# Kernel tuning notes

Measured on AMD Instinct MI355X. Metric: run time of the kernel, lower is better.

## Reference

```python
import jax, jax.numpy as jnp
import numpy as np

N_NODES = 100000
N_EDGES = 1600000
IN_DIM = 64
HIDDEN = 128
N_CLASSES = 16


def setup_inputs() -> dict:
    key = jax.random.key(0)
    ks = jax.random.split(key, 16)
    inp = {
        'feats': jax.random.normal(ks[0], (N_NODES, IN_DIM), dtype=jnp.float32),
        'H1_src': jax.random.randint(ks[1], (N_EDGES,), 0, N_NODES),
        'H1_dst': jax.random.randint(ks[2], (N_EDGES,), 0, N_NODES),
        'H2_src': jax.random.randint(ks[3], (N_EDGES,), 0, N_NODES),
        'H2_dst': jax.random.randint(ks[4], (N_EDGES,), 0, N_NODES),
        'W1_self1': 0.1 * jax.random.normal(ks[5], (IN_DIM, HIDDEN), dtype=jnp.float32),
        'W1_neigh1': 0.1 * jax.random.normal(ks[6], (IN_DIM, HIDDEN), dtype=jnp.float32),
        'W1_self2': 0.1 * jax.random.normal(ks[7], (HIDDEN, HIDDEN), dtype=jnp.float32),
        'W1_neigh2': 0.1 * jax.random.normal(ks[8], (HIDDEN, HIDDEN), dtype=jnp.float32),
        'W1_lin': 0.1 * jax.random.normal(ks[9], (HIDDEN, N_CLASSES), dtype=jnp.float32),
        'W2_self1': 0.1 * jax.random.normal(ks[10], (IN_DIM, HIDDEN), dtype=jnp.float32),
        'W2_neigh1': 0.1 * jax.random.normal(ks[11], (IN_DIM, HIDDEN), dtype=jnp.float32),
        'W2_self2': 0.1 * jax.random.normal(ks[12], (HIDDEN, HIDDEN), dtype=jnp.float32),
        'W2_neigh2': 0.1 * jax.random.normal(ks[13], (HIDDEN, HIDDEN), dtype=jnp.float32),
        'W2_lin': 0.1 * jax.random.normal(ks[14], (HIDDEN, N_CLASSES), dtype=jnp.float32),
    }
    return inp


def _neighbor_mean(x, src, dst, n_nodes):
    # gather messages along edges, sum into destinations, divide by in-degree
    msg = x[src]                                        # [E, d] irregular gather
    agg = jax.ops.segment_sum(msg, dst, num_segments=n_nodes)  # [N, d]
    deg = jax.ops.segment_sum(jnp.ones((src.shape[0],), x.dtype), dst,
                              num_segments=n_nodes)     # [N]
    return agg / jnp.maximum(deg, 1.0)[:, None]         # zero-degree nodes -> 0


def _sage_layer(x, src, dst, W_self, W_neigh):
    h_neigh = _neighbor_mean(x, src, dst, x.shape[0])
    return jax.nn.relu(x @ W_self + h_neigh @ W_neigh)


def _graphsage(src, dst, x, Ws1, Wn1, Ws2, Wn2, Wlin):
    h = _sage_layer(x, src, dst, Ws1, Wn1)
    h = _sage_layer(h, src, dst, Ws2, Wn2)
    graph_rep = jnp.mean(h, axis=0)                     # dgl.mean_nodes (single graph)
    return jax.nn.sigmoid(graph_rep @ Wlin)             # [num_classes]


def reference(feats, H1_src, H1_dst, H2_src, H2_dst,
              W1_self1, W1_neigh1, W1_self2, W1_neigh2, W1_lin,
              W2_self1, W2_neigh1, W2_self2, W2_neigh2, W2_lin):
    rep1 = _graphsage(H1_src, H1_dst, feats, W1_self1, W1_neigh1, W1_self2, W1_neigh2, W1_lin)
    rep2 = _graphsage(H2_src, H2_dst, feats, W2_self1, W2_neigh1, W2_self2, W2_neigh2, W2_lin)
    return (rep1 + rep2) / 2.0
```

## Files before the change

### kernel.cpp

```cpp
#include <hip/hip_runtime.h>
#include <hip/hip_fp16.h>

#define NN 100000
#define NE 1600000
#define IND 64
#define HID 128
#define NCLS 16
#define NGRP 3125
#define RBLK 125
#define NCRS 98
#define CAPC 18432
#define CAPF 656
#define NDCAP 48
#define EPB1 8192
#define NBG1 ((NE + EPB1 - 1) / EPB1)
#define FSPLIT 4
#define FSPAN ((CAPC + FSPLIT - 1) / FSPLIT)

typedef float v2f __attribute__((ext_vector_type(2)));
typedef __attribute__((ext_vector_type(8))) short short8v;
typedef __attribute__((ext_vector_type(4))) float f32x4;

__device__ __forceinline__ float fp8_sw_unpack(unsigned b) {
    unsigned s = (b >> 7) & 1u, em = b & 0x7fu;
    return __uint_as_float((s << 31) | (em << 20)) * 0x1p+120f;
}
__device__ __forceinline__ unsigned fp8_sw_pack(float f) {
    float c = fminf(fmaxf(f, -448.f), 448.f) * 0x1p-120f;
    unsigned b = __float_as_uint(c);
    unsigned s = b >> 31; b &= 0x7fffffffu;
    b = b + 0x7ffffu + ((b >> 20) & 1u);
    unsigned em = b >> 20;
    if (em > 0x7eu) em = 0x7eu;
    return (s << 7) | em;
}
template<bool HI>
__device__ __forceinline__ unsigned pk8(float a, float b, unsigned old) {
#if __has_builtin(__builtin_amdgcn_cvt_pk_fp8_f32)
    return (unsigned)__builtin_amdgcn_cvt_pk_fp8_f32(a, b, (int)old, HI);
#else
    unsigned v = fp8_sw_pack(a) | (fp8_sw_pack(b) << 8);
    return HI ? ((old & 0x0000ffffu) | (v << 16)) : ((old & 0xffff0000u) | v);
#endif
}
template<bool HI>
__device__ __forceinline__ v2f upk8(unsigned u) {
#if __has_builtin(__builtin_amdgcn_cvt_pk_f32_fp8)
    return __builtin_amdgcn_cvt_pk_f32_fp8((int)u, HI);
#else
    unsigned x = HI ? (u >> 16) : u;
    v2f r; r.x = fp8_sw_unpack(x & 0xffu); r.y = fp8_sw_unpack((x >> 8) & 0xffu);
    return r;
#endif
}

__device__ __forceinline__ short f2bf(float f) {
    unsigned u = __float_as_uint(f);
    return (short)((u + 0x7fffu + ((u >> 16) & 1u)) >> 16);
}

__device__ __forceinline__ void bacc8v(v2f* a, uint4 v) {
    a[0] += upk8<false>(v.x); a[1] += upk8<true>(v.x);
    a[2] += upk8<false>(v.y); a[3] += upk8<true>(v.y);
    a[4] += upk8<false>(v.z); a[5] += upk8<true>(v.z);
    a[6] += upk8<false>(v.w); a[7] += upk8<true>(v.w);
}

__device__ __forceinline__ short8v mk8(const v2f* a, float iv) {
    short8v r;
    r[0] = f2bf(a[0].x * iv); r[1] = f2bf(a[0].y * iv);
    r[2] = f2bf(a[1].x * iv); r[3] = f2bf(a[1].y * iv);
    r[4] = f2bf(a[2].x * iv); r[5] = f2bf(a[2].y * iv);
    r[6] = f2bf(a[3].x * iv); r[7] = f2bf(a[3].y * iv);
    return r;
}

__global__ void conv16_kernel(const float4* __restrict__ x, uint4* __restrict__ o, int n16) {
    int i = blockIdx.x * blockDim.x + threadIdx.x;
    if (i >= n16) return;
    float4 v0 = x[4 * i + 0], v1 = x[4 * i + 1], v2 = x[4 * i + 2], v3 = x[4 * i + 3];
    uint4 u;
    u.x = pk8<true>(v0.z, v0.w, pk8<false>(v0.x, v0.y, 0u));
    u.y = pk8<true>(v1.z, v1.w, pk8<false>(v1.x, v1.y, 0u));
    u.z = pk8<true>(v2.z, v2.w, pk8<false>(v2.x, v2.y, 0u));
    u.w = pk8<true>(v3.z, v3.w, pk8<false>(v3.x, v3.y, 0u));
    o[i] = u;
}

__global__ void packW_all(const float* __restrict__ Ws1a, const float* __restrict__ Wn1a,
                          const float* __restrict__ Ws1b, const float* __restrict__ Wn1b,
                          const float* __restrict__ Ws2a, const float* __restrict__ Wn2a,
                          const float* __restrict__ Ws2b, const float* __restrict__ Wn2b,
                          short* __restrict__ out) {
    int t = blockIdx.x * 256 + threadIdx.x;
    if (t >= 12288) return;
    const float *Ws, *Wn; short* o; int KS;
    if (t < 2048)      { Ws = Ws1a; Wn = Wn1a; o = out;         KS = 64;  }
    else if (t < 4096) { Ws = Ws1b; Wn = Wn1b; o = out + 16384; KS = 64;  t -= 2048; }
    else if (t < 8192) { Ws = Ws2a; Wn = Wn2a; o = out + 32768; KS = 128; t -= 4096; }
    else               { Ws = Ws2b; Wn = Wn2b; o = out + 65536; KS = 128; t -= 8192; }
    int l = t & 63, f = t >> 6, nn = f & 7, kk = f >> 3;
    int col = nn * 16 + (l & 15);
    int k0 = kk * 32 + ((l >> 4) * 8);
    unsigned short v[8];
#pragma unroll
    for (int j = 0; j < 8; j++) {
        int k = k0 + j;
        float x = (k < KS) ? Ws[k * 128 + col] : Wn[(k - KS) * 128 + col];
        v[j] = (unsigned short)f2bf(x);
    }
    uint4 u;
    u.x = (unsigned)v[0] | ((unsigned)v[1] << 16);
    u.y = (unsigned)v[2] | ((unsigned)v[3] << 16);
    u.z = (unsigned)v[4] | ((unsigned)v[5] << 16);
    u.w = (unsigned)v[6] | ((unsigned)v[7] << 16);
    ((uint4*)o)[t] = u;
}

__global__ __launch_bounds__(512) void place_coarse(
    const int* __restrict__ s0, const int* __restrict__ d0,
    const int* __restrict__ s1, const int* __restrict__ d1,
    int* __restrict__ gcurC,
    unsigned* __restrict__ pc0, unsigned* __restrict__ pc1) {
    __shared__ unsigned ebuf[EPB1];
    __shared__ int h[128], off[128];
    __shared__ int hb[NCRS];
    const int bi = blockIdx.x;
    const int g = bi >= NBG1;
    const int* src = g ? s1 : s0;
    const int* dst = g ? d1 : d0;
    unsigned* pc = g ? pc1 : pc0;
    const int base = (g ? bi - NBG1 : bi) * EPB1;
    const int tid = threadIdx.x;
    int nle = NE - base; if (nle > EPB1) nle = EPB1;

    if (tid < 128) h[tid] = 0;
    __syncthreads();
    for (int j = tid; j < nle; j += 512) atomicAdd(&h[dst[base + j] >> 10], 1);
    __syncthreads();
    if (tid < 128) off[tid] = h[tid];
    __syncthreads();
    for (int o = 1; o < 128; o <<= 1) {
        int v = (tid < 128 && tid >= o) ? off[tid - o] : 0;
        __syncthreads();
        if (tid < 128) off[tid] += v;
        __syncthreads();
    }
    if (tid < NCRS) hb[tid] = h[tid] ? atomicAdd(&gcurC[g * NCRS + tid], h[tid]) : 0;
    __syncthreads();
    if (tid < 128) h[tid] = off[tid] - h[tid];
    __syncthreads();
    for (int j = tid; j < nle; j += 512) {
        int d = dst[base + j];
        int b = d >> 10;
        int pos = atomicAdd(&h[b], 1);
        ebuf[pos] = (unsigned)src[base + j] | ((unsigned)(d & 1023) << 17);
    }
    __syncthreads();
    const int wv = tid >> 6, lane = tid & 63;
    for (int b = wv; b < NCRS; b += 8) {
        int beg = b ? off[b - 1] : 0;
        int run = off[b] - beg;
        int gb = hb[b];
        if (gb + run > CAPC) run = CAPC - gb;
        for (int i = lane; i < run; i += 64)
            pc[(size_t)b * CAPC + gb + i] = ebuf[beg + i];
    }
}

__global__ __launch_bounds__(512) void place_fine(
    const unsigned* __restrict__ pc0, const unsigned* __restrict__ pc1,
    const int* __restrict__ gcurC,
    unsigned* __restrict__ pf0, unsigned* __restrict__ pf1,
    int* __restrict__ fcur) {
    __shared__ unsigned obuf[FSPAN];
    __shared__ int h2[32], off2[32], cur2[32], gb2[32];
    const int bi = blockIdx.x;
    const int g = bi >= NCRS * FSPLIT;
    const int idx = g ? bi - NCRS * FSPLIT : bi;
    const int c = idx >> 2, part = idx & (FSPLIT - 1);
    const unsigned* pc = g ? pc1 : pc0;
    unsigned* pf = g ? pf1 : pf0;
    int* fc = fcur + (size_t)g * NCRS * 32;
    int ecnt = gcurC[g * NCRS + c];
    if (ecnt > CAPC) ecnt = CAPC;
    int span = (ecnt + FSPLIT - 1) / FSPLIT;
    int st = part * span;
    int en = st + span; if (en > ecnt) en = ecnt;
    int n = en - st; if (n < 0) n = 0;
    const size_t cb = (size_t)c * CAPC + st;
    const int tid = threadIdx.x;
    const int wv = tid >> 6, lane = tid & 63;

    if (tid < 32) h2[tid] = 0;
    __syncthreads();
    for (int e = tid; e < n; e += 512)
        atomicAdd(&h2[(pc[cb + e] >> 22) & 31], 1);
    __syncthreads();
    if (tid < 32) {
        gb2[tid] = h2[tid] ? atomicAdd(&fc[c * 32 + tid], h2[tid]) : 0;
        off2[tid] = h2[tid];
    }
    __syncthreads();
    for (int o = 1; o < 32; o <<= 1) {
        int v = (tid < 32 && tid >= o) ? off2[tid - o] : 0;
        __syncthreads();
        if (tid < 32) off2[tid] += v;
        __syncthreads();
    }
    if (tid < 32) cur2[tid] = off2[tid] - h2[tid];
    __syncthreads();
    for (int e = tid; e < n; e += 512) {
        unsigned u = pc[cb + e];
        int sub = (u >> 22) & 31;
        int pos = atomicAdd(&cur2[sub], 1);
        obuf[pos] = (u & 0x1FFFFu) | (((u >> 17) & 31u) << 17);
    }
    __syncthreads();
    for (int sub = wv; sub < 32; sub += 8) {
        int beg = sub ? off2[sub - 1] : 0;
        int run = off2[sub] - beg;
        int gb = gb2[sub];
        if (gb >= CAPF) run = 0;
        else if (gb + run > CAPF) run = CAPF - gb;
        for (int i = lane; i < run; i += 64)
            pf[(size_t)(c * 32 + sub) * CAPF + gb + i] = obuf[beg + i];
    }
}

template<int KS, bool REDUCE>
__global__ __launch_bounds__(512) void sage_fused(
    const float* __restrict__ xin,
    const unsigned* __restrict__ x8a, const unsigned* __restrict__ x8b,
    const unsigned* __restrict__ pf0, const unsigned* __restrict__ pf1,
    const int* __restrict__ fcur,
    const short* __restrict__ Wfa, const short* __restrict__ Wfb,
    float* __restrict__ outRa, float* __restrict__ outRb,
    unsigned* __restrict__ outHa, unsigned* __restrict__ outHb) {
    constexpr int KT = (2 * KS) / 32;
    __shared__ short8v sA[KT * 128];
    __shared__ float otile[REDUCE ? 1 : 32 * 132];
    __shared__ int lcnt[32];
    __shared__ int ssrcL[32 * NDCAP];

    const int tid = threadIdx.x;
    const int g = blockIdx.x >= NGRP;
    const int gid = g ? blockIdx.x - NGRP : blockIdx.x;
    const int n0 = gid * 32;
    const unsigned* x8 = g ? x8b : x8a;
    const unsigned* pf = g ? pf1 : pf0;
    const int* fc = fcur + (size_t)g * NCRS * 32;
    const short8v* Wf = (const short8v*)(g ? Wfb : Wfa);
    const uint4* xb4 = (const uint4*)x8;

    if (tid < 32) lcnt[tid] = 0;
    __syncthreads();

    {
        int ecnt = fc[gid];
        if (ecnt > CAPF) ecnt = CAPF;
        for (int e = tid; e < ecnt; e += 512) {
            unsigned u = pf[(size_t)gid * CAPF + e];
            int loc = (u >> 17) & 31;
            int pos = atomicAdd(&lcnt[loc], 1);
            if (pos < NDCAP) ssrcL[loc * NDCAP + pos] = (int)(u & 0x1FFFFu);
        }
    }

    if (tid < 256) {
        if constexpr (KS == IND) {
            int node = tid >> 3, r = tid & 7;
            float4 v0 = ((const float4*)xin)[(size_t)(n0 + node) * 16 + r * 2];
            float4 v1 = ((const float4*)xin)[(size_t)(n0 + node) * 16 + r * 2 + 1];
            short8v s;
            s[0] = f2bf(v0.x); s[1] = f2bf(v0.y); s[2] = f2bf(v0.z); s[3] = f2bf(v0.w);
            s[4] = f2bf(v1.x); s[5] = f2bf(v1.y); s[6] = f2bf(v1.z); s[7] = f2bf(v1.w);
            int kk = r >> 2, kg = r & 3;
            sA[(kk * 128 + (node >> 4) * 64 + kg * 16 + (node & 15)) ^ (kk & 7)] = s;
        } else {
            int node = tid >> 3, c8 = tid & 7;
            uint4 u = xb4[(size_t)(n0 + node) * 8 + c8];
            v2f a[8];
            a[0] = upk8<false>(u.x); a[1] = upk8<true>(u.x);
            a[2] = upk8<false>(u.y); a[3] = upk8<true>(u.y);
            a[4] = upk8<false>(u.z); a[5] = upk8<true>(u.z);
            a[6] = upk8<false>(u.w); a[7] = upk8<true>(u.w);
            int kk = c8 >> 1, kg0 = (c8 & 1) * 2;
            int tb = (node >> 4) * 64, nl = node & 15;
            sA[(kk * 128 + tb + kg0 * 16 + nl) ^ (kk & 7)]       = mk8(a, 1.0f);
            sA[(kk * 128 + tb + (kg0 + 1) * 16 + nl) ^ (kk & 7)] = mk8(a + 4, 1.0f);
        }
    }
    __syncthreads();

    {
        const int nb = tid >> 4;
        const int degt = lcnt[nb];
        const int degc = degt > NDCAP ? NDCAP : degt;
        const int* L = &ssrcL[nb * NDCAP];
        const int tb = (nb >> 4) * 64, nl = nb & 15;
        v2f a[8];
#pragma unroll
        for (int j = 0; j < 8; j++) a[j] = (v2f)(0.0f);

        if constexpr (KS == HID) {
            const int l = tid & 7;
            const int h = (tid >> 3) & 1;
            int i = h;
            for (; i + 2 < degc; i += 4) {
                int i0 = L[i], i1 = L[i + 2];
                uint4 v0 = xb4[(size_t)i0 * 8 + l];
                uint4 v1 = xb4[(size_t)i1 * 8 + l];
                bacc8v(a, v0);
                bacc8v(a, v1);
            }
            if (i < degc) bacc8v(a, xb4[(size_t)L[i] * 8 + l]);
#pragma unroll
            for (int j = 0; j < 8; j++) {
                a[j].x += __shfl_xor(a[j].x, 8);
                a[j].y += __shfl_xor(a[j].y, 8);
            }
            if (h == 0) {
                float iv = 1.0f / fmaxf((float)degt, 1.0f);
                int kk = 4 + (l >> 1), kg0 = (l & 1) * 2;
                sA[(kk * 128 + tb + kg0 * 16 + nl) ^ (kk & 7)]       = mk8(a, iv);
                sA[(kk * 128 + tb + (kg0 + 1) * 16 + nl) ^ (kk & 7)] = mk8(a + 4, iv);
            }
        } else {
            const int sub = tid & 15;
            const int l = sub & 3;
            const int h = sub >> 2;
            int i = h;
            for (; i + 4 < degc; i += 8) {
                int i0 = L[i], i1 = L[i + 4];
                uint4 v0 = xb4[(size_t)i0 * 4 + l];
                uint4 v1 = xb4[(size_t)i1 * 4 + l];
                bacc8v(a, v0);
                bacc8v(a, v1);
            }
            if (i < degc) bacc8v(a, xb4[(size_t)L[i] * 4 + l]);
#pragma unroll
            for (int j = 0; j < 8; j++) {
                a[j].x += __shfl_xor(a[j].x, 4);
                a[j].y += __shfl_xor(a[j].y, 4);
            }
#pragma unroll
            for (int j = 0; j < 8; j++) {
                a[j].x += __shfl_xor(a[j].x, 8);
                a[j].y += __shfl_xor(a[j].y, 8);
            }
            if (h == 0) {
                float iv = 1.0f / fmaxf((float)degt, 1.0f);
                int kk = 2 + (l >> 1), kg0 = (l & 1) * 2;
                sA[(kk * 128 + tb + kg0 * 16 + nl) ^ (kk & 7)]       = mk8(a, iv);
                sA[(kk * 128 + tb + (kg0 + 1) * 16 + nl) ^ (kk & 7)] = mk8(a + 4, iv);
            }
        }
    }
    __syncthreads();

    const int lane = tid & 63;
    const int q = tid >> 6;
    const int r15 = lane & 15;
    const int kg = lane >> 4;
    f32x4 acc0 = {0.f, 0.f, 0.f, 0.f};
    f32x4 acc1 = {0.f, 0.f, 0.f, 0.f};

#pragma unroll
    for (int kk = 0; kk < KT; kk++) {
        short8v af0 = sA[(kk * 128 + lane) ^ (kk & 7)];
        short8v af1 = sA[(kk * 128 + 64 + lane) ^ (kk & 7)];
        short8v b0 = Wf[(kk * 8 + q) * 64 + lane];
        acc0 = __builtin_amdgcn_mfma_f32_16x16x32_bf16(af0, b0, acc0, 0, 0, 0);
        acc1 = __builtin_amdgcn_mfma_f32_16x16x32_bf16(af1, b0, acc1, 0, 0, 0);
    }

    if constexpr (!REDUCE) {
#pragma unroll
        for (int i = 0; i < 4; i++) {
            otile[(kg * 4 + i) * 132 + 16 * q + r15]        = fmaxf(acc0[i], 0.f);
            otile[(16 + kg * 4 + i) * 132 + 16 * q + r15]   = fmaxf(acc1[i], 0.f);
        }
        __syncthreads();
        int node = tid >> 4, c = tid & 15;
        float4 x0 = *(const float4*)&otile[node * 132 + c * 8];
        float4 x1 = *(const float4*)&otile[node * 132 + c * 8 + 4];
        unsigned w0 = pk8<false>(x0.x, x0.y, 0u); w0 = pk8<true>(x0.z, x0.w, w0);
        unsigned w1 = pk8<false>(x1.x, x1.y, 0u); w1 = pk8<true>(x1.z, x1.w, w1);
        uint2* o8 = (uint2*)(g ? outHb : outHa);
        o8[(size_t)(n0 + node) * 16 + c] = make_uint2(w0, w1);
    } else {
        float s0 = 0.f;
#pragma unroll
        for (int i = 0; i < 4; i++)
            s0 += fmaxf(acc0[i], 0.f) + fmaxf(acc1[i], 0.f);
        s0 += __shfl_xor(s0, 16); s0 += __shfl_xor(s0, 32);
        float* outR = g ? outRb : outRa;
        if (lane < 16) outR[(size_t)gid * 128 + 16 * q + lane] = s0;
    }
}

__global__ void reduce1_kernel(const float* __restrict__ p0, const float* __restrict__ p1,
                               float* __restrict__ p2) {
    const int bb = blockIdx.x;
    const int tid = threadIdx.x;
    const int g = tid >> 7;
    const int col = tid & 127;
    const float* p = g ? p1 : p0;
    const int per = NGRP / RBLK;
    float s = 0.0f;
    for (int r = 0; r < per; r++) s += p[(size_t)(bb * per + r) * 128 + col];
    p2[(size_t)bb * 256 + tid] = s;
}

__global__ void final_kernel(const float* __restrict__ p2,
                             const float* __restrict__ Wlin1,
                             const float* __restrict__ Wlin2,
                             float* __restrict__ out) {
    __shared__ float rep[2][HID];
    __shared__ float sg[32];
    const int tid = threadIdx.x;
    float s = 0.0f;
    for (int r = 0; r < RBLK; r++) s += p2[r * 256 + tid];
    rep[tid >> 7][tid & 127] = s * (1.0f / (float)NN);
    __syncthreads();
    if (tid < 32) {
        const int g = tid / 16;
        const int c = tid % 16;
        const float* W = g ? Wlin2 : Wlin1;
        float a = 0.0f;
        for (int k = 0; k < HID; k++) a += rep[g][k] * W[k * NCLS + c];
        sg[tid] = 1.0f / (1.0f + expf(-a));
    }
    __syncthreads();
    if (tid < 16) out[tid] = 0.5f * (sg[tid] + sg[16 + tid]);
}

extern "C" void kernel_launch(void* const* d_in, const int* in_sizes, int n_in,
                              void* d_out, int out_size, void* d_ws, size_t ws_size,
                              hipStream_t stream) {
    const float* feats = (const float*)d_in[0];
    const int* srcp[2] = {(const int*)d_in[1], (const int*)d_in[3]};
    const int* dstp[2] = {(const int*)d_in[2], (const int*)d_in[4]};
    const float* Ws1[2] = {(const float*)d_in[5], (const float*)d_in[10]};
    const float* Wn1[2] = {(const float*)d_in[6], (const float*)d_in[11]};
    const float* Ws2[2] = {(const float*)d_in[7], (const float*)d_in[12]};
    const float* Wn2[2] = {(const float*)d_in[8], (const float*)d_in[13]};
    const float* Wlin[2] = {(const float*)d_in[9], (const float*)d_in[14]};

    const size_t PFN = (size_t)NCRS * 32 * CAPF;
    char* w = (char*)d_ws;
    unsigned* fb8 = (unsigned*)w;   w += (size_t)NN * IND;
    unsigned* h18a = (unsigned*)w;  w += (size_t)NN * HID;
    unsigned* h18b = (unsigned*)w;  w += (size_t)NN * HID;
    unsigned* pf0 = (unsigned*)w;   w += PFN * 4;
    unsigned* pf1 = (unsigned*)w;   w += PFN * 4;
    float* part0 = (float*)w;       w += (size_t)NGRP * 128 * 4;
    float* part1 = (float*)w;       w += (size_t)NGRP * 128 * 4;
    float* p2 = (float*)w;          w += (size_t)RBLK * 256 * 4;
    int* fcur = (int*)w;            w += (size_t)2 * NCRS * 32 * 4;
    int* gcurC = (int*)w;           w += 2 * NCRS * 4;
    w = (char*)(((uintptr_t)w + 15) & ~(uintptr_t)15);
    short* wpk = (short*)w;         w += 98304 * 2;
    unsigned* pc0 = h18a;
    unsigned* pc1 = h18b;

    conv16_kernel<<<(NN * IND / 16 + 255) / 256, 256, 0, stream>>>(
        (const float4*)feats, (uint4*)fb8, NN * IND / 16);

    packW_all<<<48, 256, 0, stream>>>(Ws1[0], Wn1[0], Ws1[1], Wn1[1],
                                      Ws2[0], Wn2[0], Ws2[1], Wn2[1], wpk);

    (void)hipMemsetAsync(gcurC, 0, 2 * NCRS * 4, stream);
    (void)hipMemsetAsync(fcur, 0, (size_t)2 * NCRS * 32 * 4, stream);
    place_coarse<<<2 * NBG1, 512, 0, stream>>>(srcp[0], dstp[0], srcp[1], dstp[1],
                                               gcurC, pc0, pc1);
    place_fine<<<2 * NCRS * FSPLIT, 512, 0, stream>>>(pc0, pc1, gcurC, pf0, pf1, fcur);

    sage_fused<IND, false><<<2 * NGRP, 512, 0, stream>>>(
        feats, fb8, fb8, pf0, pf1, fcur,
        wpk, wpk + 16384,
        nullptr, nullptr, h18a, h18b);

    sage_fused<HID, true><<<2 * NGRP, 512, 0, stream>>>(
        nullptr, h18a, h18b, pf0, pf1, fcur,
        wpk + 32768, wpk + 65536,
        part0, part1, nullptr, nullptr);

    reduce1_kernel<<<RBLK, 256, 0, stream>>>(part0, part1, p2);
    final_kernel<<<1, 256, 0, stream>>>(p2, Wlin[0], Wlin[1], (float*)d_out);
}
```

Measured before the change: 280.4 us.

## Double nodes per block to 64, widen blocks to 1024 threads, fuse prep kernels

Each SAGE block now processes 64 destination nodes with 1024 threads instead of 32 nodes with 512. To match, the fine bucketing is regrouped into 16 sub-buckets per coarse bucket, with larger per-bucket capacity and more blocks per coarse bucket in place_fine. The feature conversion, weight packing and counter zeroing are merged into one prep kernel, which removes two launches and two memsets. The layer-2 partial sums are reduced in shared memory before the store, and tail guards are added because the node count no longer divides evenly. The trade-off is more shared memory per block and fewer resident blocks, which may lower latency hiding in the gather phase.

```diff
diff --git a/kernel.cpp b/kernel.cpp
--- a/kernel.cpp
+++ b/kernel.cpp
@@ -6,16 +6,20 @@
 #define IND 64
 #define HID 128
 #define NCLS 16
-#define NGRP 3125
-#define RBLK 125
+#define NPB 64
+#define NGRP 1563
+#define RBLK 128
+#define RPER 13
 #define NCRS 98
 #define CAPC 18432
-#define CAPF 656
+#define CAPF 1216
 #define NDCAP 48
 #define EPB1 8192
 #define NBG1 ((NE + EPB1 - 1) / EPB1)
-#define FSPLIT 4
+#define FSPLIT 8
 #define FSPAN ((CAPC + FSPLIT - 1) / FSPLIT)
+#define CONVB 1563
+#define PACKB 48
 
 typedef float v2f __attribute__((ext_vector_type(2)));
 typedef __attribute__((ext_vector_type(8))) short short8v;
@@ -75,49 +79,55 @@
     return r;
 }
 
-__global__ void conv16_kernel(const float4* __restrict__ x, uint4* __restrict__ o, int n16) {
-    int i = blockIdx.x * blockDim.x + threadIdx.x;
-    if (i >= n16) return;
-    float4 v0 = x[4 * i + 0], v1 = x[4 * i + 1], v2 = x[4 * i + 2], v3 = x[4 * i + 3];
-    uint4 u;
-    u.x = pk8<true>(v0.z, v0.w, pk8<false>(v0.x, v0.y, 0u));
-    u.y = pk8<true>(v1.z, v1.w, pk8<false>(v1.x, v1.y, 0u));
-    u.z = pk8<true>(v2.z, v2.w, pk8<false>(v2.x, v2.y, 0u));
-    u.w = pk8<true>(v3.z, v3.w, pk8<false>(v3.x, v3.y, 0u));
-    o[i] = u;
-}
-
-__global__ void packW_all(const float* __restrict__ Ws1a, const float* __restrict__ Wn1a,
-                          const float* __restrict__ Ws1b, const float* __restrict__ Wn1b,
-                          const float* __restrict__ Ws2a, const float* __restrict__ Wn2a,
-                          const float* __restrict__ Ws2b, const float* __restrict__ Wn2b,
-                          short* __restrict__ out) {
-    int t = blockIdx.x * 256 + threadIdx.x;
-    if (t >= 12288) return;
-    const float *Ws, *Wn; short* o; int KS;
-    if (t < 2048)      { Ws = Ws1a; Wn = Wn1a; o = out;         KS = 64;  }
-    else if (t < 4096) { Ws = Ws1b; Wn = Wn1b; o = out + 16384; KS = 64;  t -= 2048; }
-    else if (t < 8192) { Ws = Ws2a; Wn = Wn2a; o = out + 32768; KS = 128; t -= 4096; }
-    else               { Ws = Ws2b; Wn = Wn2b; o = out + 65536; KS = 128; t -= 8192; }
-    int l = t & 63, f = t >> 6, nn = f & 7, kk = f >> 3;
-    int col = nn * 16 + (l & 15);
-    int k0 = kk * 32 + ((l >> 4) * 8);
-    unsigned short v[8];
-#pragma unroll
-    for (int j = 0; j < 8; j++) {
-        int k = k0 + j;
-        float x = (k < KS) ? Ws[k * 128 + col] : Wn[(k - KS) * 128 + col];
-        v[j] = (unsigned short)f2bf(x);
-    }
-    uint4 u;
-    u.x = (unsigned)v[0] | ((unsigned)v[1] << 16);
-    u.y = (unsigned)v[2] | ((unsigned)v[3] << 16);
-    u.z = (unsigned)v[4] | ((unsigned)v[5] << 16);
-    u.w = (unsigned)v[6] | ((unsigned)v[7] << 16);
-    ((uint4*)o)[t] = u;
-}
-
-__global__ __launch_bounds__(512) void place_coarse(
+__global__ __launch_bounds__(256) void prep_kernel(
+    const float4* __restrict__ x, uint4* __restrict__ o8,
+    const float* __restrict__ Ws1a, const float* __restrict__ Wn1a,
+    const float* __restrict__ Ws1b, const float* __restrict__ Wn1b,
+    const float* __restrict__ Ws2a, const float* __restrict__ Wn2a,
+    const float* __restrict__ Ws2b, const float* __restrict__ Wn2b,
+    short* __restrict__ out, int* __restrict__ gcurC, int* __restrict__ fcur) {
+    const int bi = blockIdx.x;
+    if (bi < CONVB) {
+        int i = bi * 256 + threadIdx.x;
+        if (i >= NN * IND / 16) return;
+        float4 v0 = x[4 * i + 0], v1 = x[4 * i + 1], v2 = x[4 * i + 2], v3 = x[4 * i + 3];
+        uint4 u;
+        u.x = pk8<true>(v0.z, v0.w, pk8<false>(v0.x, v0.y, 0u));
+        u.y = pk8<true>(v1.z, v1.w, pk8<false>(v1.x, v1.y, 0u));
+        u.z = pk8<true>(v2.z, v2.w, pk8<false>(v2.x, v2.y, 0u));
+        u.w = pk8<true>(v3.z, v3.w, pk8<false>(v3.x, v3.y, 0u));
+        o8[i] = u;
+    } else if (bi < CONVB + PACKB) {
+        int t = (bi - CONVB) * 256 + threadIdx.x;
+        if (t >= 12288) return;
+        const float *Ws, *Wn; short* o; int KS;
+        if (t < 2048)      { Ws = Ws1a; Wn = Wn1a; o = out;         KS = 64;  }
+        else if (t < 4096) { Ws = Ws1b; Wn = Wn1b; o = out + 16384; KS = 64;  t -= 2048; }
+        else if (t < 8192) { Ws = Ws2a; Wn = Wn2a; o = out + 32768; KS = 128; t -= 4096; }
+        else               { Ws = Ws2b; Wn = Wn2b; o = out + 65536; KS = 128; t -= 8192; }
+        int l = t & 63, f = t >> 6, nn = f & 7, kk = f >> 3;
+        int col = nn * 16 + (l & 15);
+        int k0 = kk * 32 + ((l >> 4) * 8);
+        unsigned short v[8];
+#pragma unroll
+        for (int j = 0; j < 8; j++) {
+            int k = k0 + j;
+            float xx = (k < KS) ? Ws[k * 128 + col] : Wn[(k - KS) * 128 + col];
+            v[j] = (unsigned short)f2bf(xx);
+        }
+        uint4 u;
+        u.x = (unsigned)v[0] | ((unsigned)v[1] << 16);
+        u.y = (unsigned)v[2] | ((unsigned)v[3] << 16);
+        u.z = (unsigned)v[4] | ((unsigned)v[5] << 16);
+        u.w = (unsigned)v[6] | ((unsigned)v[7] << 16);
+        ((uint4*)o)[t] = u;
+    } else {
+        for (int i = threadIdx.x; i < 2 * NCRS * 16; i += 256) fcur[i] = 0;
+        for (int i = threadIdx.x; i < 2 * NCRS; i += 256) gcurC[i] = 0;
+    }
+}
+
+__global__ __launch_bounds__(1024) void place_coarse(
     const int* __restrict__ s0, const int* __restrict__ d0,
     const int* __restrict__ s1, const int* __restrict__ d1,
     int* __restrict__ gcurC,
@@ -136,7 +146,7 @@
 
     if (tid < 128) h[tid] = 0;
     __syncthreads();
-    for (int j = tid; j < nle; j += 512) atomicAdd(&h[dst[base + j] >> 10], 1);
+    for (int j = tid; j < nle; j += 1024) atomicAdd(&h[dst[base + j] >> 10], 1);
     __syncthreads();
     if (tid < 128) off[tid] = h[tid];
     __syncthreads();
@@ -150,7 +160,7 @@
     __syncthreads();
     if (tid < 128) h[tid] = off[tid] - h[tid];
     __syncthreads();
-    for (int j = tid; j < nle; j += 512) {
+    for (int j = tid; j < nle; j += 1024) {
         int d = dst[base + j];
         int b = d >> 10;
         int pos = atomicAdd(&h[b], 1);
@@ -158,7 +168,7 @@
     }
     __syncthreads();
     const int wv = tid >> 6, lane = tid & 63;
-    for (int b = wv; b < NCRS; b += 8) {
+    for (int b = wv; b < NCRS; b += 16) {
         int beg = b ? off[b - 1] : 0;
         int run = off[b] - beg;
         int gb = hb[b];
@@ -168,20 +178,20 @@
     }
 }
 
-__global__ __launch_bounds__(512) void place_fine(
+__global__ __launch_bounds__(1024) void place_fine(
     const unsigned* __restrict__ pc0, const unsigned* __restrict__ pc1,
     const int* __restrict__ gcurC,
     unsigned* __restrict__ pf0, unsigned* __restrict__ pf1,
     int* __restrict__ fcur) {
     __shared__ unsigned obuf[FSPAN];
-    __shared__ int h2[32], off2[32], cur2[32], gb2[32];
+    __shared__ int h2[16], off2[16], cur2[16], gb2[16];
     const int bi = blockIdx.x;
     const int g = bi >= NCRS * FSPLIT;
     const int idx = g ? bi - NCRS * FSPLIT : bi;
-    const int c = idx >> 2, part = idx & (FSPLIT - 1);
+    const int c = idx >> 3, part = idx & (FSPLIT - 1);
     const unsigned* pc = g ? pc1 : pc0;
     unsigned* pf = g ? pf1 : pf0;
-    int* fc = fcur + (size_t)g * NCRS * 32;
+    int* fc = fcur + (size_t)g * NCRS * 16;
     int ecnt = gcurC[g * NCRS + c];
     if (ecnt > CAPC) ecnt = CAPC;
     int span = (ecnt + FSPLIT - 1) / FSPLIT;
@@ -192,44 +202,44 @@
     const int tid = threadIdx.x;
     const int wv = tid >> 6, lane = tid & 63;
 
-    if (tid < 32) h2[tid] = 0;
-    __syncthreads();
-    for (int e = tid; e < n; e += 512)
-        atomicAdd(&h2[(pc[cb + e] >> 22) & 31], 1);
-    __syncthreads();
-    if (tid < 32) {
-        gb2[tid] = h2[tid] ? atomicAdd(&fc[c * 32 + tid], h2[tid]) : 0;
+    if (tid < 16) h2[tid] = 0;
+    __syncthreads();
+    for (int e = tid; e < n; e += 1024)
+        atomicAdd(&h2[(pc[cb + e] >> 23) & 15], 1);
+    __syncthreads();
+    if (tid < 16) {
+        gb2[tid] = h2[tid] ? atomicAdd(&fc[c * 16 + tid], h2[tid]) : 0;
         off2[tid] = h2[tid];
     }
     __syncthreads();
-    for (int o = 1; o < 32; o <<= 1) {
-        int v = (tid < 32 && tid >= o) ? off2[tid - o] : 0;
+    for (int o = 1; o < 16; o <<= 1) {
+        int v = (tid < 16 && tid >= o) ? off2[tid - o] : 0;
         __syncthreads();
-        if (tid < 32) off2[tid] += v;
+        if (tid < 16) off2[tid] += v;
         __syncthreads();
     }
-    if (tid < 32) cur2[tid] = off2[tid] - h2[tid];
-    __syncthreads();
-    for (int e = tid; e < n; e += 512) {
+    if (tid < 16) cur2[tid] = off2[tid] - h2[tid];
+    __syncthreads();
+    for (int e = tid; e < n; e += 1024) {
         unsigned u = pc[cb + e];
-        int sub = (u >> 22) & 31;
+        int sub = (u >> 23) & 15;
         int pos = atomicAdd(&cur2[sub], 1);
-        obuf[pos] = (u & 0x1FFFFu) | (((u >> 17) & 31u) << 17);
-    }
-    __syncthreads();
-    for (int sub = wv; sub < 32; sub += 8) {
+        obuf[pos] = (u & 0x1FFFFu) | (((u >> 17) & 63u) << 17);
+    }
+    __syncthreads();
+    for (int sub = wv; sub < 16; sub += 16) {
         int beg = sub ? off2[sub - 1] : 0;
         int run = off2[sub] - beg;
         int gb = gb2[sub];
         if (gb >= CAPF) run = 0;
         else if (gb + run > CAPF) run = CAPF - gb;
         for (int i = lane; i < run; i += 64)
-            pf[(size_t)(c * 32 + sub) * CAPF + gb + i] = obuf[beg + i];
+            pf[(size_t)(c * 16 + sub) * CAPF + gb + i] = obuf[beg + i];
     }
 }
 
 template<int KS, bool REDUCE>
-__global__ __launch_bounds__(512) void sage_fused(
+__global__ __launch_bounds__(1024) void sage_fused(
     const float* __restrict__ xin,
     const unsigned* __restrict__ x8a, const unsigned* __restrict__ x8b,
     const unsigned* __restrict__ pf0, const unsigned* __restrict__ pf1,
@@ -238,48 +248,52 @@
     float* __restrict__ outRa, float* __restrict__ outRb,
     unsigned* __restrict__ outHa, unsigned* __restrict__ outHb) {
     constexpr int KT = (2 * KS) / 32;
-    __shared__ short8v sA[KT * 128];
-    __shared__ float otile[REDUCE ? 1 : 32 * 132];
-    __shared__ int lcnt[32];
-    __shared__ int ssrcL[32 * NDCAP];
+    __shared__ short8v sA[KT * 256];
+    __shared__ float otile[REDUCE ? 2 * 128 : NPB * 132];
+    __shared__ int lcnt[NPB];
+    __shared__ int ssrcL[NPB * NDCAP];
 
     const int tid = threadIdx.x;
     const int g = blockIdx.x >= NGRP;
     const int gid = g ? blockIdx.x - NGRP : blockIdx.x;
-    const int n0 = gid * 32;
+    const int n0 = gid * NPB;
     const unsigned* x8 = g ? x8b : x8a;
     const unsigned* pf = g ? pf1 : pf0;
-    const int* fc = fcur + (size_t)g * NCRS * 32;
+    const int* fc = fcur + (size_t)g * NCRS * 16;
     const short8v* Wf = (const short8v*)(g ? Wfb : Wfa);
     const uint4* xb4 = (const uint4*)x8;
 
-    if (tid < 32) lcnt[tid] = 0;
+    if (tid < NPB) lcnt[tid] = 0;
     __syncthreads();
 
     {
         int ecnt = fc[gid];
         if (ecnt > CAPF) ecnt = CAPF;
-        for (int e = tid; e < ecnt; e += 512) {
+        for (int e = tid; e < ecnt; e += 1024) {
             unsigned u = pf[(size_t)gid * CAPF + e];
-            int loc = (u >> 17) & 31;
+            int loc = (u >> 17) & 63;
             int pos = atomicAdd(&lcnt[loc], 1);
             if (pos < NDCAP) ssrcL[loc * NDCAP + pos] = (int)(u & 0x1FFFFu);
         }
     }
 
-    if (tid < 256) {
+    if (tid < 512) {
+        int node = tid >> 3;
+        bool ok = (n0 + node) < NN;
         if constexpr (KS == IND) {
-            int node = tid >> 3, r = tid & 7;
-            float4 v0 = ((const float4*)xin)[(size_t)(n0 + node) * 16 + r * 2];
-            float4 v1 = ((const float4*)xin)[(size_t)(n0 + node) * 16 + r * 2 + 1];
+            int r = tid & 7;
+            float4 v0 = ok ? ((const float4*)xin)[(size_t)(n0 + node) * 16 + r * 2]
+                           : make_float4(0.f, 0.f, 0.f, 0.f);
+            float4 v1 = ok ? ((const float4*)xin)[(size_t)(n0 + node) * 16 + r * 2 + 1]
+                           : make_float4(0.f, 0.f, 0.f, 0.f);
             short8v s;
             s[0] = f2bf(v0.x); s[1] = f2bf(v0.y); s[2] = f2bf(v0.z); s[3] = f2bf(v0.w);
             s[4] = f2bf(v1.x); s[5] = f2bf(v1.y); s[6] = f2bf(v1.z); s[7] = f2bf(v1.w);
             int kk = r >> 2, kg = r & 3;
-            sA[(kk * 128 + (node >> 4) * 64 + kg * 16 + (node & 15)) ^ (kk & 7)] = s;
+            sA[(kk * 256 + (node >> 4) * 64 + kg * 16 + (node & 15)) ^ (kk & 7)] = s;
         } else {
-            int node = tid >> 3, c8 = tid & 7;
-            uint4 u = xb4[(size_t)(n0 + node) * 8 + c8];
+            int c8 = tid & 7;
+            uint4 u = ok ? xb4[(size_t)(n0 + node) * 8 + c8] : make_uint4(0, 0, 0, 0);
             v2f a[8];
             a[0] = upk8<false>(u.x); a[1] = upk8<true>(u.x);
             a[2] = upk8<false>(u.y); a[3] = upk8<true>(u.y);
@@ -287,8 +301,8 @@
             a[6] = upk8<false>(u.w); a[7] = upk8<true>(u.w);
             int kk = c8 >> 1, kg0 = (c8 & 1) * 2;
             int tb = (node >> 4) * 64, nl = node & 15;
-            sA[(kk * 128 + tb + kg0 * 16 + nl) ^ (kk & 7)]       = mk8(a, 1.0f);
-            sA[(kk * 128 + tb + (kg0 + 1) * 16 + nl) ^ (kk & 7)] = mk8(a + 4, 1.0f);
+            sA[(kk * 256 + tb + kg0 * 16 + nl) ^ (kk & 7)]       = mk8(a, 1.0f);
+            sA[(kk * 256 + tb + (kg0 + 1) * 16 + nl) ^ (kk & 7)] = mk8(a + 4, 1.0f);
         }
     }
     __syncthreads();
@@ -323,8 +337,8 @@
             if (h == 0) {
                 float iv = 1.0f / fmaxf((float)degt, 1.0f);
                 int kk = 4 + (l >> 1), kg0 = (l & 1) * 2;
-                sA[(kk * 128 + tb + kg0 * 16 + nl) ^ (kk & 7)]       = mk8(a, iv);
-                sA[(kk * 128 + tb + (kg0 + 1) * 16 + nl) ^ (kk & 7)] = mk8(a + 4, iv);
+                sA[(kk * 256 + tb + kg0 * 16 + nl) ^ (kk & 7)]       = mk8(a, iv);
+                sA[(kk * 256 + tb + (kg0 + 1) * 16 + nl) ^ (kk & 7)] = mk8(a + 4, iv);
             }
         } else {
             const int sub = tid & 15;
@@ -352,8 +366,8 @@
             if (h == 0) {
                 float iv = 1.0f / fmaxf((float)degt, 1.0f);
                 int kk = 2 + (l >> 1), kg0 = (l & 1) * 2;
-                sA[(kk * 128 + tb + kg0 * 16 + nl) ^ (kk & 7)]       = mk8(a, iv);
-                sA[(kk * 128 + tb + (kg0 + 1) * 16 + nl) ^ (kk & 7)] = mk8(a + 4, iv);
+                sA[(kk * 256 + tb + kg0 * 16 + nl) ^ (kk & 7)]       = mk8(a, iv);
+                sA[(kk * 256 + tb + (kg0 + 1) * 16 + nl) ^ (kk & 7)] = mk8(a + 4, iv);
             }
         }
     }
@@ -363,14 +377,15 @@
     const int q = tid >> 6;
     const int r15 = lane & 15;
     const int kg = lane >> 4;
+    const int ct = q & 7, rt = q >> 3;
     f32x4 acc0 = {0.f, 0.f, 0.f, 0.f};
     f32x4 acc1 = {0.f, 0.f, 0.f, 0.f};
 
 #pragma unroll
     for (int kk = 0; kk < KT; kk++) {
-        short8v af0 = sA[(kk * 128 + lane) ^ (kk & 7)];
-        short8v af1 = sA[(kk * 128 + 64 + lane) ^ (kk & 7)];
-        short8v b0 = Wf[(kk * 8 + q) * 64 + lane];
+        short8v af0 = sA[(kk * 256 + rt * 128 + lane) ^ (kk & 7)];
+        short8v af1 = sA[(kk * 256 + rt * 128 + 64 + lane) ^ (kk & 7)];
+        short8v b0 = Wf[(kk * 8 + ct) * 64 + lane];
         acc0 = __builtin_amdgcn_mfma_f32_16x16x32_bf16(af0, b0, acc0, 0, 0, 0);
         acc1 = __builtin_amdgcn_mfma_f32_16x16x32_bf16(af1, b0, acc1, 0, 0, 0);
     }
@@ -378,25 +393,31 @@
     if constexpr (!REDUCE) {
 #pragma unroll
         for (int i = 0; i < 4; i++) {
-            otile[(kg * 4 + i) * 132 + 16 * q + r15]        = fmaxf(acc0[i], 0.f);
-            otile[(16 + kg * 4 + i) * 132 + 16 * q + r15]   = fmaxf(acc1[i], 0.f);
+            otile[(rt * 32 + kg * 4 + i) * 132 + 16 * ct + r15]      = fmaxf(acc0[i], 0.f);
+            otile[(rt * 32 + 16 + kg * 4 + i) * 132 + 16 * ct + r15] = fmaxf(acc1[i], 0.f);
         }
         __syncthreads();
         int node = tid >> 4, c = tid & 15;
-        float4 x0 = *(const float4*)&otile[node * 132 + c * 8];
-        float4 x1 = *(const float4*)&otile[node * 132 + c * 8 + 4];
-        unsigned w0 = pk8<false>(x0.x, x0.y, 0u); w0 = pk8<true>(x0.z, x0.w, w0);
-        unsigned w1 = pk8<false>(x1.x, x1.y, 0u); w1 = pk8<true>(x1.z, x1.w, w1);
-        uint2* o8 = (uint2*)(g ? outHb : outHa);
-        o8[(size_t)(n0 + node) * 16 + c] = make_uint2(w0, w1);
+        if (n0 + node < NN) {
+            float4 x0 = *(const float4*)&otile[node * 132 + c * 8];
+            float4 x1 = *(const float4*)&otile[node * 132 + c * 8 + 4];
+            unsigned w0 = pk8<false>(x0.x, x0.y, 0u); w0 = pk8<true>(x0.z, x0.w, w0);
+            unsigned w1 = pk8<false>(x1.x, x1.y, 0u); w1 = pk8<true>(x1.z, x1.w, w1);
+            uint2* o8 = (uint2*)(g ? outHb : outHa);
+            o8[(size_t)(n0 + node) * 16 + c] = make_uint2(w0, w1);
+        }
     } else {
         float s0 = 0.f;
 #pragma unroll
         for (int i = 0; i < 4; i++)
             s0 += fmaxf(acc0[i], 0.f) + fmaxf(acc1[i], 0.f);
         s0 += __shfl_xor(s0, 16); s0 += __shfl_xor(s0, 32);
-        float* outR = g ? outRb : outRa;
-        if (lane < 16) outR[(size_t)gid * 128 + 16 * q + lane] = s0;
+        if (lane < 16) otile[rt * 128 + 16 * ct + lane] = s0;
+        __syncthreads();
+        if (tid < 128) {
+            float* outR = g ? outRb : outRa;
+            outR[(size_t)gid * 128 + tid] = otile[tid] + otile[128 + tid];
+        }
     }
 }
 
@@ -407,9 +428,11 @@
     const int g = tid >> 7;
     const int col = tid & 127;
     const float* p = g ? p1 : p0;
-    const int per = NGRP / RBLK;
     float s = 0.0f;
-    for (int r = 0; r < per; r++) s += p[(size_t)(bb * per + r) * 128 + col];
+    for (int r = 0; r < RPER; r++) {
+        int idx = bb * RPER + r;
+        if (idx < NGRP) s += p[(size_t)idx * 128 + col];
+    }
     p2[(size_t)bb * 256 + tid] = s;
 }
 
@@ -448,7 +471,7 @@
     const float* Wn2[2] = {(const float*)d_in[8], (const float*)d_in[13]};
     const float* Wlin[2] = {(const float*)d_in[9], (const float*)d_in[14]};
 
-    const size_t PFN = (size_t)NCRS * 32 * CAPF;
+    const size_t PFN = (size_t)NCRS * 16 * CAPF;
     char* w = (char*)d_ws;
     unsigned* fb8 = (unsigned*)w;   w += (size_t)NN * IND;
     unsigned* h18a = (unsigned*)w;  w += (size_t)NN * HID;
@@ -458,31 +481,28 @@
     float* part0 = (float*)w;       w += (size_t)NGRP * 128 * 4;
     float* part1 = (float*)w;       w += (size_t)NGRP * 128 * 4;
     float* p2 = (float*)w;          w += (size_t)RBLK * 256 * 4;
-    int* fcur = (int*)w;            w += (size_t)2 * NCRS * 32 * 4;
+    int* fcur = (int*)w;            w += (size_t)2 * NCRS * 16 * 4;
     int* gcurC = (int*)w;           w += 2 * NCRS * 4;
     w = (char*)(((uintptr_t)w + 15) & ~(uintptr_t)15);
     short* wpk = (short*)w;         w += 98304 * 2;
     unsigned* pc0 = h18a;
     unsigned* pc1 = h18b;
 
-    conv16_kernel<<<(NN * IND / 16 + 255) / 256, 256, 0, stream>>>(
-        (const float4*)feats, (uint4*)fb8, NN * IND / 16);
-
-    packW_all<<<48, 256, 0, stream>>>(Ws1[0], Wn1[0], Ws1[1], Wn1[1],
-                                      Ws2[0], Wn2[0], Ws2[1], Wn2[1], wpk);
-
-    (void)hipMemsetAsync(gcurC, 0, 2 * NCRS * 4, stream);
-    (void)hipMemsetAsync(fcur, 0, (size_t)2 * NCRS * 32 * 4, stream);
-    place_coarse<<<2 * NBG1, 512, 0, stream>>>(srcp[0], dstp[0], srcp[1], dstp[1],
-                                               gcurC, pc0, pc1);
-    place_fine<<<2 * NCRS * FSPLIT, 512, 0, stream>>>(pc0, pc1, gcurC, pf0, pf1, fcur);
-
-    sage_fused<IND, false><<<2 * NGRP, 512, 0, stream>>>(
+    prep_kernel<<<CONVB + PACKB + 1, 256, 0, stream>>>(
+        (const float4*)feats, (uint4*)fb8,
+        Ws1[0], Wn1[0], Ws1[1], Wn1[1],
+        Ws2[0], Wn2[0], Ws2[1], Wn2[1], wpk, gcurC, fcur);
+
+    place_coarse<<<2 * NBG1, 1024, 0, stream>>>(srcp[0], dstp[0], srcp[1], dstp[1],
+                                                gcurC, pc0, pc1);
+    place_fine<<<2 * NCRS * FSPLIT, 1024, 0, stream>>>(pc0, pc1, gcurC, pf0, pf1, fcur);
+
+    sage_fused<IND, false><<<2 * NGRP, 1024, 0, stream>>>(
         feats, fb8, fb8, pf0, pf1, fcur,
         wpk, wpk + 16384,
         nullptr, nullptr, h18a, h18b);
 
-    sage_fused<HID, true><<<2 * NGRP, 512, 0, stream>>>(
+    sage_fused<HID, true><<<2 * NGRP, 1024, 0, stream>>>(
         nullptr, h18a, h18b, pf0, pf1, fcur,
         wpk + 32768, wpk + 65536,
         part0, part1, nullptr, nullptr);
```

Measured after the change: 290.7 us. 3.7% more time.
